# Optimization experiments

Measured on AMD Instinct MI355X. Metric: run time of the kernel, lower is better.

The kernel has to match this reference:

```python
import jax, jax.numpy as jnp
import numpy as np

CHANNELS = 256
L = 8192


def setup_inputs() -> dict:
    key = jax.random.key(0)
    ks = jax.random.split(key, 7)
    s = 1.0 / np.sqrt(CHANNELS)
    return {
        "x": jax.random.normal(ks[0], (L, CHANNELS), dtype=jnp.float32),
        "Wq": jax.random.normal(ks[1], (CHANNELS, CHANNELS), dtype=jnp.float32) * s,
        "bq": jax.random.normal(ks[2], (CHANNELS,), dtype=jnp.float32) * s,
        "Wk": jax.random.normal(ks[3], (CHANNELS, CHANNELS), dtype=jnp.float32) * s,
        "bk": jax.random.normal(ks[4], (CHANNELS,), dtype=jnp.float32) * s,
        "Wv": jax.random.normal(ks[5], (CHANNELS, CHANNELS), dtype=jnp.float32) * s,
        "bv": jax.random.normal(ks[6], (CHANNELS,), dtype=jnp.float32) * s,
    }


def reference(x, Wq, bq, Wk, bk, Wv, bv):
    # x: [L, C] (already flat). Linear: y = x @ W.T + b
    x2 = x.reshape(-1, CHANNELS)
    l = x2.shape[0]
    q = x2 @ Wq.T + bq          # [L, C]
    k = x2 @ Wk.T + bk          # [L, C]
    v = x2 @ Wv.T + bv          # [L, C]
    attn = q @ k.T              # [L, L]
    # torch: attn / sqrt(attn.numel()) = attn / sqrt(L*L) = attn / L
    attn = attn / jnp.float32(l)
    # GLOBAL softmax over the entire flattened L*L matrix
    attn = jax.nn.softmax(attn.reshape(-1), axis=0).reshape(l, l)
    return attn @ v             # [L, C]
```

## Files before the change

kernel.cpp:

```cpp
#include <hip/hip_runtime.h>

#define LSEQ 8192
#define CH   256

typedef __attribute__((ext_vector_type(8)))  short short8;
typedef __attribute__((ext_vector_type(4)))  short short4v;
typedef __attribute__((ext_vector_type(16))) float f32x16;
typedef unsigned int u32;

__device__ inline short f2bf(float f) {
  union { float f; unsigned u; } v; v.f = f;
  unsigned r = v.u + 0x7fffu + ((v.u >> 16) & 1u);
  return (short)(r >> 16);
}
__device__ inline short8 cvt8(float4 a, float4 b) {
  short8 v;
  v[0] = f2bf(a.x); v[1] = f2bf(a.y); v[2] = f2bf(a.z); v[3] = f2bf(a.w);
  v[4] = f2bf(b.x); v[5] = f2bf(b.y); v[6] = f2bf(b.z); v[7] = f2bf(b.w);
  return v;
}
__device__ inline f32x16 mfma32(short8 a, short8 b, f32x16 c) {
  return __builtin_amdgcn_mfma_f32_32x32x16_bf16(a, b, c, 0, 0, 0);
}
__device__ __forceinline__ void gload16(const void* g, void* l) {
  __builtin_amdgcn_global_load_lds(
      (const __attribute__((address_space(1))) u32*)g,
      (__attribute__((address_space(3))) u32*)l, 16, 0, 0);
}

__global__ __launch_bounds__(256) void qkv_kernel(
    const float* __restrict__ x,
    const float* __restrict__ Wq, const float* __restrict__ bq,
    const float* __restrict__ Wk, const float* __restrict__ bk,
    const float* __restrict__ Wv, const float* __restrict__ bv,
    short* __restrict__ Qb, short* __restrict__ KTb, short* __restrict__ VTb,
    float* __restrict__ sums)
{
  const int m = blockIdx.y;
  const float* W  = (m == 0) ? Wq : ((m == 1) ? Wk : Wv);
  const float* bp = (m == 0) ? bq : ((m == 1) ? bk : bv);
  const int rb = blockIdx.x >> 1, cb = blockIdx.x & 1;
  const int row0 = rb * 128, col0 = cb * 128;

  __shared__ __align__(16) short wt[128 * 256];
  __shared__ float colred[4][128];

  const int tid = threadIdx.x;
#pragma unroll
  for (int i = 0; i < 16; ++i) {
    int g = i * 256 + tid;
    int rr = g >> 5, p = g & 31;
    const float4* src = (const float4*)(W + (col0 + rr) * CH + ((p ^ (rr & 31)) * 8));
    short8 v = cvt8(src[0], src[1]);
    *(short8*)(&wt[rr * 256 + p * 8]) = v;
  }
  __syncthreads();

  const int wid = tid >> 6, lane = tid & 63, l31 = lane & 31, hi = lane >> 5;
  const int wrow0 = row0 + wid * 32;

  f32x16 acc[4] = {};
#pragma unroll
  for (int kd = 0; kd < 16; ++kd) {
    const float4* xs = (const float4*)(x + (size_t)(wrow0 + l31) * CH + kd * 16 + hi * 8);
    short8 af = cvt8(xs[0], xs[1]);
#pragma unroll
    for (int nf = 0; nf < 4; ++nf) {
      int r = nf * 32 + l31;
      short8 bf = *(const short8*)(&wt[r * 256 + (((kd * 2 + hi) ^ (r & 31)) * 8)]);
      acc[nf] = mfma32(af, bf, acc[nf]);
    }
  }

#pragma unroll
  for (int nf = 0; nf < 4; ++nf) {
    int col = col0 + nf * 32 + l31;
    float bias = bp[col];
    float cs = 0.f;
    if (m == 0) {
#pragma unroll
      for (int r = 0; r < 16; ++r) {
        float y = acc[nf][r] + bias;
        cs += y;
        int row = wrow0 + (r & 3) + 8 * (r >> 2) + 4 * hi;
        Qb[(size_t)row * CH + col] = f2bf(y);
      }
    } else {
      short* dst = (m == 1) ? KTb : VTb;
#pragma unroll
      for (int g = 0; g < 4; ++g) {
        short4v v;
#pragma unroll
        for (int r2 = 0; r2 < 4; ++r2) {
          float y = acc[nf][g * 4 + r2] + bias;
          cs += y;
          v[r2] = f2bf(y);
        }
        *(short4v*)(&dst[(size_t)col * LSEQ + wrow0 + g * 8 + hi * 4]) = v;
      }
    }
    cs += __shfl_xor(cs, 32);
    if (hi == 0) colred[wid][nf * 32 + l31] = cs;
  }
  __syncthreads();
  if (tid < 128) {
    float s = colred[0][tid] + colred[1][tid] + colred[2][tid] + colred[3][tid];
    atomicAdd(&sums[m * CH + col0 + tid], s);
  }
}

__global__ __launch_bounds__(256) void gram_kernel(
    const short* __restrict__ VTb, const short* __restrict__ KTb,
    float* __restrict__ MT)
{
  __shared__ __align__(16) short at[128 * 128];
  __shared__ __align__(16) short bt[128 * 128];

  const int tile = blockIdx.x & 3, split = blockIdx.x >> 2;
  const int d0 = (tile >> 1) * 128, c0 = (tile & 1) * 128;
  const int tid = threadIdx.x, wid = tid >> 6, lane = tid & 63;
  const int l31 = lane & 31, hi = lane >> 5;
  const int wr = wid >> 1, wc = wid & 1;

  f32x16 acc[2][2] = {};

#pragma unroll
  for (int jj = 0; jj < 2; ++jj) {
    const int j0 = split * 256 + jj * 128;
    __syncthreads();
#pragma unroll
    for (int i = 0; i < 8; ++i) {
      int g = i * 256 + tid, rr = g >> 4, p = g & 15;
      gload16(VTb + (size_t)(d0 + rr) * LSEQ + j0 + ((p ^ (rr & 15)) * 8),
              &at[(i * 256 + wid * 64) * 8]);
    }
#pragma unroll
    for (int i = 0; i < 8; ++i) {
      int g = i * 256 + tid, rr = g >> 4, p = g & 15;
      gload16(KTb + (size_t)(c0 + rr) * LSEQ + j0 + ((p ^ (rr & 15)) * 8),
              &bt[(i * 256 + wid * 64) * 8]);
    }
    __syncthreads();

#pragma unroll
    for (int kd = 0; kd < 8; ++kd) {
      int ra0 = wr * 64 + l31, ra1 = ra0 + 32;
      int rb0 = wc * 64 + l31, rb1 = rb0 + 32;
      int ck = kd * 2 + hi;
      short8 a0 = *(const short8*)(&at[ra0 * 128 + ((ck ^ (ra0 & 15)) * 8)]);
      short8 a1 = *(const short8*)(&at[ra1 * 128 + ((ck ^ (ra1 & 15)) * 8)]);
      short8 b0 = *(const short8*)(&bt[rb0 * 128 + ((ck ^ (rb0 & 15)) * 8)]);
      short8 b1 = *(const short8*)(&bt[rb1 * 128 + ((ck ^ (rb1 & 15)) * 8)]);
      acc[0][0] = mfma32(a0, b0, acc[0][0]);
      acc[0][1] = mfma32(a0, b1, acc[0][1]);
      acc[1][0] = mfma32(a1, b0, acc[1][0]);
      acc[1][1] = mfma32(a1, b1, acc[1][1]);
    }
  }

#pragma unroll
  for (int mt = 0; mt < 2; ++mt)
#pragma unroll
    for (int nt = 0; nt < 2; ++nt) {
      int ccol = c0 + wc * 64 + nt * 32 + l31;
#pragma unroll
      for (int r = 0; r < 16; ++r) {
        int r2 = r ^ (split & 15);
        int drow = d0 + wr * 64 + mt * 32 + (r2 & 3) + 8 * (r2 >> 2) + 4 * hi;
        atomicAdd(&MT[drow * CH + ccol], acc[mt][nt][r2]);
      }
    }
}

__global__ __launch_bounds__(256) void final_kernel(
    const short* __restrict__ Qb, const float* __restrict__ MT,
    const float* __restrict__ sums, float* __restrict__ out)
{
  __shared__ __align__(16) short wt[128 * 256];
  __shared__ float zs[256];

  const int tid = threadIdx.x;
  zs[tid] = sums[tid] * sums[CH + tid];
  __syncthreads();
#pragma unroll
  for (int st = 128; st > 0; st >>= 1) {
    if (tid < st) zs[tid] += zs[tid + st];
    __syncthreads();
  }
  const float Zinv = 1.0f / (67108864.0f + zs[0] * (1.0f / 8192.0f));

  const int rb = blockIdx.x >> 1, cb = blockIdx.x & 1;
  const int row0 = rb * 128, col0 = cb * 128;

#pragma unroll
  for (int i = 0; i < 16; ++i) {
    int g = i * 256 + tid;
    int rr = g >> 5, p = g & 31;
    const float4* src = (const float4*)(MT + (col0 + rr) * CH + ((p ^ (rr & 31)) * 8));
    short8 v = cvt8(src[0], src[1]);
    *(short8*)(&wt[rr * 256 + p * 8]) = v;
  }
  __syncthreads();

  const int wid = tid >> 6, lane = tid & 63, l31 = lane & 31, hi = lane >> 5;
  const int wrow0 = row0 + wid * 32;

  short8 qf[16];
#pragma unroll
  for (int kd = 0; kd < 16; ++kd)
    qf[kd] = *(const short8*)(Qb + (size_t)(wrow0 + l31) * CH + kd * 16 + hi * 8);

  f32x16 acc[4] = {};
#pragma unroll
  for (int kd = 0; kd < 16; ++kd)
#pragma unroll
    for (int nf = 0; nf < 4; ++nf) {
      int r = nf * 32 + l31;
      short8 bf = *(const short8*)(&wt[r * 256 + (((kd * 2 + hi) ^ (r & 31)) * 8)]);
      acc[nf] = mfma32(qf[kd], bf, acc[nf]);
    }

  const float* colsum = sums + 2 * CH;
#pragma unroll
  for (int nf = 0; nf < 4; ++nf) {
    int col = col0 + nf * 32 + l31;
    float cs = colsum[col];
#pragma unroll
    for (int r = 0; r < 16; ++r) {
      int row = wrow0 + (r & 3) + 8 * (r >> 2) + 4 * hi;
      out[(size_t)row * CH + col] = (cs + acc[nf][r] * (1.0f / 8192.0f)) * Zinv;
    }
  }
}

extern "C" void kernel_launch(void* const* d_in, const int* in_sizes, int n_in,
                              void* d_out, int out_size, void* d_ws, size_t ws_size,
                              hipStream_t stream) {
  const float* x  = (const float*)d_in[0];
  const float* Wq = (const float*)d_in[1];
  const float* bq = (const float*)d_in[2];
  const float* Wk = (const float*)d_in[3];
  const float* bk = (const float*)d_in[4];
  const float* Wv = (const float*)d_in[5];
  const float* bv = (const float*)d_in[6];
  float* out = (float*)d_out;

  char* ws = (char*)d_ws;
  short* Qb  = (short*)ws;
  short* KTb = Qb  + (size_t)LSEQ * CH;
  short* VTb = KTb + (size_t)CH * LSEQ;
  float* MT   = (float*)(VTb + (size_t)CH * LSEQ);
  float* sums = MT + (size_t)CH * CH;

  hipMemsetAsync(MT, 0, (size_t)CH * CH * sizeof(float) + 3 * CH * sizeof(float),
                 stream);

  qkv_kernel<<<dim3(128, 3), 256, 0, stream>>>(x, Wq, bq, Wk, bk, Wv, bv,
                                               Qb, KTb, VTb, sums);
  gram_kernel<<<128, 256, 0, stream>>>(VTb, KTb, MT);
  final_kernel<<<128, 256, 0, stream>>>(Qb, MT, sums, out);
}
```

Measured before the change: 46.50 us.

## Drop memset and atomics; zero MT in qkv kernel, deterministic partial-sum reduction

Removes the hipMemsetAsync by having the Q-projection blocks zero the MT accumulator. Column-sum atomics are replaced by per-row-block partial sums, which one extra gram block reduces into a scalar table read by the final kernel. Gram splits are halved (64 blocks, each covering 512 of the sequence), which halves the atomic traffic into MT but leaves fewer blocks on the GPU. The intent is to cut one launch and atomic contention, at the cost of lower gram parallelism and a serial reduction block.

```diff
diff --git a/kernel.cpp b/kernel.cpp
--- a/kernel.cpp
+++ b/kernel.cpp
@@ -34,7 +34,7 @@
     const float* __restrict__ Wk, const float* __restrict__ bk,
     const float* __restrict__ Wv, const float* __restrict__ bv,
     short* __restrict__ Qb, short* __restrict__ KTb, short* __restrict__ VTb,
-    float* __restrict__ sums)
+    float* __restrict__ sp, float* __restrict__ MT)
 {
   const int m = blockIdx.y;
   const float* W  = (m == 0) ? Wq : ((m == 1) ? Wk : Wv);
@@ -46,6 +46,12 @@
   __shared__ float colred[4][128];
 
   const int tid = threadIdx.x;
+
+  if (m == 0 && tid < 128) {
+    float4 z = {0.f, 0.f, 0.f, 0.f};
+    ((float4*)(MT + (size_t)blockIdx.x * 512))[tid] = z;
+  }
+
 #pragma unroll
   for (int i = 0; i < 16; ++i) {
     int g = i * 256 + tid;
@@ -105,28 +111,51 @@
   __syncthreads();
   if (tid < 128) {
     float s = colred[0][tid] + colred[1][tid] + colred[2][tid] + colred[3][tid];
-    atomicAdd(&sums[m * CH + col0 + tid], s);
+    sp[((size_t)m * 64 + rb) * 256 + col0 + tid] = s;
   }
 }
 
 __global__ __launch_bounds__(256) void gram_kernel(
     const short* __restrict__ VTb, const short* __restrict__ KTb,
-    float* __restrict__ MT)
+    const float* __restrict__ sp, float* __restrict__ MT,
+    float* __restrict__ scal)
 {
   __shared__ __align__(16) short at[128 * 128];
   __shared__ __align__(16) short bt[128 * 128];
 
+  const int tid = threadIdx.x;
+
+  if (blockIdx.x == 64) {
+    float s0 = 0.f, s1 = 0.f, s2 = 0.f;
+    for (int rb = 0; rb < 64; ++rb) {
+      s0 += sp[(size_t)(0 * 64 + rb) * 256 + tid];
+      s1 += sp[(size_t)(1 * 64 + rb) * 256 + tid];
+      s2 += sp[(size_t)(2 * 64 + rb) * 256 + tid];
+    }
+    scal[1 + tid] = s2;
+    float* red = (float*)at;
+    red[tid] = s0 * s1;
+    __syncthreads();
+#pragma unroll
+    for (int st = 128; st > 0; st >>= 1) {
+      if (tid < st) red[tid] += red[tid + st];
+      __syncthreads();
+    }
+    if (tid == 0) scal[0] = red[0];
+    return;
+  }
+
   const int tile = blockIdx.x & 3, split = blockIdx.x >> 2;
   const int d0 = (tile >> 1) * 128, c0 = (tile & 1) * 128;
-  const int tid = threadIdx.x, wid = tid >> 6, lane = tid & 63;
+  const int wid = tid >> 6, lane = tid & 63;
   const int l31 = lane & 31, hi = lane >> 5;
   const int wr = wid >> 1, wc = wid & 1;
 
   f32x16 acc[2][2] = {};
 
 #pragma unroll
-  for (int jj = 0; jj < 2; ++jj) {
-    const int j0 = split * 256 + jj * 128;
+  for (int jj = 0; jj < 4; ++jj) {
+    const int j0 = split * 512 + jj * 128;
     __syncthreads();
 #pragma unroll
     for (int i = 0; i < 8; ++i) {
@@ -174,20 +203,12 @@
 
 __global__ __launch_bounds__(256) void final_kernel(
     const short* __restrict__ Qb, const float* __restrict__ MT,
-    const float* __restrict__ sums, float* __restrict__ out)
+    const float* __restrict__ scal, float* __restrict__ out)
 {
   __shared__ __align__(16) short wt[128 * 256];
-  __shared__ float zs[256];
 
   const int tid = threadIdx.x;
-  zs[tid] = sums[tid] * sums[CH + tid];
-  __syncthreads();
-#pragma unroll
-  for (int st = 128; st > 0; st >>= 1) {
-    if (tid < st) zs[tid] += zs[tid + st];
-    __syncthreads();
-  }
-  const float Zinv = 1.0f / (67108864.0f + zs[0] * (1.0f / 8192.0f));
+  const float Zinv = 1.0f / (67108864.0f + scal[0] * (1.0f / 8192.0f));
 
   const int rb = blockIdx.x >> 1, cb = blockIdx.x & 1;
   const int row0 = rb * 128, col0 = cb * 128;
@@ -220,11 +241,10 @@
       acc[nf] = mfma32(qf[kd], bf, acc[nf]);
     }
 
-  const float* colsum = sums + 2 * CH;
 #pragma unroll
   for (int nf = 0; nf < 4; ++nf) {
     int col = col0 + nf * 32 + l31;
-    float cs = colsum[col];
+    float cs = scal[1 + col];
 #pragma unroll
     for (int r = 0; r < 16; ++r) {
       int row = wrow0 + (r & 3) + 8 * (r >> 2) + 4 * hi;
@@ -250,13 +270,11 @@
   short* KTb = Qb  + (size_t)LSEQ * CH;
   short* VTb = KTb + (size_t)CH * LSEQ;
   float* MT   = (float*)(VTb + (size_t)CH * LSEQ);
-  float* sums = MT + (size_t)CH * CH;
-
-  hipMemsetAsync(MT, 0, (size_t)CH * CH * sizeof(float) + 3 * CH * sizeof(float),
-                 stream);
+  float* sp   = MT + (size_t)CH * CH;
+  float* scal = sp + (size_t)3 * 64 * 256;
 
   qkv_kernel<<<dim3(128, 3), 256, 0, stream>>>(x, Wq, bq, Wk, bk, Wv, bv,
-                                               Qb, KTb, VTb, sums);
-  gram_kernel<<<128, 256, 0, stream>>>(VTb, KTb, MT);
-  final_kernel<<<128, 256, 0, stream>>>(Qb, MT, sums, out);
-}
+                                               Qb, KTb, VTb, sp, MT);
+  gram_kernel<<<65, 256, 0, stream>>>(VTb, KTb, sp, MT, scal);
+  final_kernel<<<128, 256, 0, stream>>>(Qb, MT, scal, out);
+}
```

Measured after the change: 39.31 us. 15.5% less time.
